# Kernel optimization log

Measured on AMD Instinct MI355X. Metric: run time of the kernel, lower is better.

## Reference

```python
import jax, jax.numpy as jnp
import numpy as np

N = 100000  # num_nodes

def spmm(idx, val, x):
    # sparse [N,N] (COO: idx=[2,E], val=[E]) times dense x [N,F]
    rows, cols = idx[0], idx[1]
    return jax.ops.segment_sum(val[:, None] * x[cols], rows, num_segments=N)


def setup_inputs() -> dict:
    key = jax.random.key(0)
    ks = jax.random.split(key, 12)
    E = 3200000
    F_in, F_out = 128, 128
    inp = {
        "x": jax.random.normal(ks[0], (N, F_in), dtype=jnp.float32),
        "weight": jax.random.normal(ks[1], (F_in, F_out), dtype=jnp.float32) * (1.0 / np.sqrt(F_in)),
        "filter1": 0.9 + 0.2 * jax.random.uniform(ks[2], (N, 1), dtype=jnp.float32),
        "filter2": 0.9 + 0.2 * jax.random.uniform(ks[3], (N, 1), dtype=jnp.float32),
        "filter3": 0.9 + 0.2 * jax.random.uniform(ks[4], (N, 1), dtype=jnp.float32),
        "idx1": jax.random.randint(ks[5], (2, E), 0, N, dtype=jnp.int32),
        "val1": jax.random.normal(ks[6], (E,), dtype=jnp.float32) * 0.01,
        "idx2": jax.random.randint(ks[7], (2, E), 0, N, dtype=jnp.int32),
        "val2": jax.random.normal(ks[8], (E,), dtype=jnp.float32) * 0.01,
        "idx3": jax.random.randint(ks[9], (2, E), 0, N, dtype=jnp.int32),
        "val3": jax.random.normal(ks[10], (E,), dtype=jnp.float32) * 0.01,
    }
    return inp


def reference(x, weight, filter1, filter2, filter3, idx1, val1, idx2, val2, idx3, val3):
    # x = x @ W
    x = x @ weight
    # framelet transform: three spmm branches
    x1 = spmm(idx1, val1, x)
    x2 = spmm(idx2, val2, x)
    x3 = spmm(idx3, val3, x)
    # shrinkage is None -> no-op
    # elementwise learned filters
    x1 = filter1 * x1
    x2 = filter2 * x2
    x3 = filter3 * x3
    # inverse framelet transform
    x1 = spmm(idx1, val1, x1)
    x2 = spmm(idx2, val2, x2)
    x3 = spmm(idx3, val3, x3)
    return x1 + x2 + x3
```

## Files before the change

### kernel.cpp

```cpp
#include <hip/hip_runtime.h>
#include <hip/hip_bf16.h>


#define CHUNK 4096
#define CITER 16
#define MAXC 256

typedef __attribute__((ext_vector_type(8))) short short8;
typedef __attribute__((ext_vector_type(4))) float f32x4;

static __device__ __forceinline__ unsigned short bf16bits(float v) {
  return __builtin_bit_cast(unsigned short, __float2bfloat16(v));
}
static __device__ __forceinline__ float bflo(unsigned u) {
  return __uint_as_float(u << 16);
}
static __device__ __forceinline__ float bfhi(unsigned u) {
  return __uint_as_float(u & 0xffff0000u);
}

__global__ __launch_bounds__(256) void gemm_mfma(const float* __restrict__ x,
                                                 const float* __restrict__ w,
                                                 unsigned short* __restrict__ y,
                                                 int n) {
  __shared__ unsigned short wt[128][136];
  const int tid = threadIdx.x;
#pragma unroll
  for (int it = 0; it < 16; ++it) {
    int i = it * 256 + tid;
    int k = i >> 5;
    int c4 = (i & 31) << 2;
    float4 v = ((const float4*)w)[i];
    wt[c4 + 0][k] = bf16bits(v.x);
    wt[c4 + 1][k] = bf16bits(v.y);
    wt[c4 + 2][k] = bf16bits(v.z);
    wt[c4 + 3][k] = bf16bits(v.w);
  }
  __syncthreads();
  const int lane = tid & 63, wid = tid >> 6;
  const int lr = lane & 15, lq = lane >> 4;
  const int rowbase = blockIdx.x * 128 + wid * 32;
  f32x4 acc[2][8] = {};
#pragma unroll
  for (int ks = 0; ks < 4; ++ks) {
    short8 a[2];
#pragma unroll
    for (int s = 0; s < 2; ++s) {
      int r = rowbase + s * 16 + lr;
      float4 v0 = {0.f, 0.f, 0.f, 0.f}, v1 = {0.f, 0.f, 0.f, 0.f};
      if (r < n) {
        const float* xp = x + (size_t)r * 128 + ks * 32 + lq * 8;
        v0 = *(const float4*)xp;
        v1 = *(const float4*)(xp + 4);
      }
      a[s][0] = bf16bits(v0.x);
      a[s][1] = bf16bits(v0.y);
      a[s][2] = bf16bits(v0.z);
      a[s][3] = bf16bits(v0.w);
      a[s][4] = bf16bits(v1.x);
      a[s][5] = bf16bits(v1.y);
      a[s][6] = bf16bits(v1.z);
      a[s][7] = bf16bits(v1.w);
    }
#pragma unroll
    for (int cs = 0; cs < 8; ++cs) {
      short8 b = *(const short8*)&wt[cs * 16 + lr][ks * 32 + lq * 8];
      acc[0][cs] =
          __builtin_amdgcn_mfma_f32_16x16x32_bf16(a[0], b, acc[0][cs], 0, 0, 0);
      acc[1][cs] =
          __builtin_amdgcn_mfma_f32_16x16x32_bf16(a[1], b, acc[1][cs], 0, 0, 0);
    }
  }
#pragma unroll
  for (int s = 0; s < 2; ++s) {
#pragma unroll
    for (int cs = 0; cs < 8; ++cs) {
      int col = cs * 16 + lr;
      int r0 = rowbase + s * 16 + lq * 4;
#pragma unroll
      for (int j = 0; j < 4; ++j) {
        int r = r0 + j;
        if (r < n) y[(size_t)r * 128 + col] = bf16bits(acc[s][cs][j]);
      }
    }
  }
}

__global__ void ginit(int* __restrict__ gcur, int NC, int CAP) {
  int i = blockIdx.x * 256 + threadIdx.x;
  if (i < NC) gcur[i] = i * CAP;
}

__global__ __launch_bounds__(256) void scatter1(const int* __restrict__ rows,
                                                const int* __restrict__ cols,
                                                const float* __restrict__ vals,
                                                int* __restrict__ gcur,
                                                int2* __restrict__ st1, int E,
                                                int NC) {
  __shared__ int lh[MAXC], gb[MAXC], lc[MAXC];
  __shared__ int rc[CHUNK];
  const int tid = threadIdx.x;
  lh[tid] = 0;
  __syncthreads();
  const int base = blockIdx.x * CHUNK;
#pragma unroll
  for (int k = 0; k < CITER; ++k) {
    int e = base + k * 256 + tid;
    int r = -1;
    if (e < E) {
      r = __builtin_nontemporal_load(rows + e);
      atomicAdd(&lh[r >> 9], 1);
    }
    rc[k * 256 + tid] = r;
  }
  __syncthreads();
  if (tid < NC) {
    int n = lh[tid];
    gb[tid] = n ? atomicAdd(&gcur[tid], n) : 0;
    lc[tid] = 0;
  }
  __syncthreads();
#pragma unroll
  for (int k = 0; k < CITER; ++k) {
    int e = base + k * 256 + tid;
    int r = rc[k * 256 + tid];
    if (r >= 0) {
      int c = r >> 9;
      int off = atomicAdd(&lc[c], 1);
      int2 o;
      o.x = ((r & 511) << 17) | __builtin_nontemporal_load(cols + e);
      o.y = __float_as_int(__builtin_nontemporal_load(vals + e));
      st1[gb[c] + off] = o;
    }
  }
}

__global__ __launch_bounds__(512) void scatter2(const int* __restrict__ gcur,
                                                const int2* __restrict__ st1,
                                                int2* __restrict__ st2,
                                                int2* __restrict__ rowse,
                                                int CAP) {
  __shared__ int sh[512], cur[512];
  const int c = blockIdx.x, tid = threadIdx.x;
  const int a = c * CAP;
  const int b = gcur[c];
  sh[tid] = 0;
  __syncthreads();
  for (int e = a + tid; e < b; e += 512)
    atomicAdd(&sh[(st1[e].x >> 17) & 511], 1);
  __syncthreads();
  int v = sh[tid];
  __syncthreads();
  for (int o = 1; o < 512; o <<= 1) {
    int t2 = (tid >= o) ? sh[tid - o] : 0;
    __syncthreads();
    sh[tid] += t2;
    __syncthreads();
  }
  int end = a + sh[tid];
  int start = end - v;
  cur[tid] = start;
  rowse[c * 512 + tid] = make_int2(start, end);
  __syncthreads();
  for (int e = a + tid; e < b; e += 512) {
    int2 d = st1[e];
    int r = (d.x >> 17) & 511;
    int p = atomicAdd(&cur[r], 1);
    st2[p] = make_int2(d.x & 0x1FFFF, d.y);
  }
}

static __device__ __forceinline__ void row_dot(
    int e, int e1, const int2* __restrict__ edges,
    const unsigned short* __restrict__ src, unsigned loff, float& a0,
    float& a1) {
  for (; e + 7 < e1; e += 8) {
    int4 p0 = *(const int4*)&edges[e];
    int4 p1 = *(const int4*)&edges[e + 2];
    int4 p2 = *(const int4*)&edges[e + 4];
    int4 p3 = *(const int4*)&edges[e + 6];
    unsigned u0 = *(const unsigned*)(src + (((size_t)p0.x) << 7) + loff);
    unsigned u1 = *(const unsigned*)(src + (((size_t)p0.z) << 7) + loff);
    unsigned u2 = *(const unsigned*)(src + (((size_t)p1.x) << 7) + loff);
    unsigned u3 = *(const unsigned*)(src + (((size_t)p1.z) << 7) + loff);
    unsigned u4 = *(const unsigned*)(src + (((size_t)p2.x) << 7) + loff);
    unsigned u5 = *(const unsigned*)(src + (((size_t)p2.z) << 7) + loff);
    unsigned u6 = *(const unsigned*)(src + (((size_t)p3.x) << 7) + loff);
    unsigned u7 = *(const unsigned*)(src + (((size_t)p3.z) << 7) + loff);
    float v0 = __int_as_float(p0.y), v1 = __int_as_float(p0.w);
    float v2 = __int_as_float(p1.y), v3 = __int_as_float(p1.w);
    float v4 = __int_as_float(p2.y), v5 = __int_as_float(p2.w);
    float v6 = __int_as_float(p3.y), v7 = __int_as_float(p3.w);
    a0 += v0 * bflo(u0);
    a1 += v0 * bfhi(u0);
    a0 += v1 * bflo(u1);
    a1 += v1 * bfhi(u1);
    a0 += v2 * bflo(u2);
    a1 += v2 * bfhi(u2);
    a0 += v3 * bflo(u3);
    a1 += v3 * bfhi(u3);
    a0 += v4 * bflo(u4);
    a1 += v4 * bfhi(u4);
    a0 += v5 * bflo(u5);
    a1 += v5 * bfhi(u5);
    a0 += v6 * bflo(u6);
    a1 += v6 * bfhi(u6);
    a0 += v7 * bflo(u7);
    a1 += v7 * bfhi(u7);
  }
  for (; e < e1; ++e) {
    int2 d = edges[e];
    unsigned u = *(const unsigned*)(src + (((size_t)d.x) << 7) + loff);
    float v = __int_as_float(d.y);
    a0 += v * bflo(u);
    a1 += v * bfhi(u);
  }
}

template <int MID>
__global__ __launch_bounds__(256) void spmm_w(
    const int2* __restrict__ rowse, const int2* __restrict__ edges,
    const unsigned short* __restrict__ src, unsigned short* __restrict__ dst,
    float* __restrict__ out, const float* __restrict__ filt, int N, int accm) {
  const int lane = threadIdx.x & 63, wid = threadIdx.x >> 6;
  const int row = blockIdx.x * 4 + wid;
  if (row >= N) return;
  const int2 se = rowse[row];
  float a0 = 0.f, a1 = 0.f;
  const unsigned loff = (unsigned)(lane << 1);
  row_dot(se.x, se.y, edges, src, loff, a0, a1);
  if (MID) {
    float fl = filt[row];
    a0 *= fl;
    a1 *= fl;
    unsigned o = (unsigned)bf16bits(a0) | ((unsigned)bf16bits(a1) << 16);
    *(unsigned*)(dst + ((size_t)row << 7) + loff) = o;
  } else {
    float* op = out + ((size_t)row << 7) + loff;
    float2 r;
    r.x = a0;
    r.y = a1;
    if (accm) {
      float2 c = *(const float2*)op;
      r.x += c.x;
      r.y += c.y;
    }
    *(float2*)op = r;
  }
}

__global__ __launch_bounds__(256) void spmm_out3(
    const int2* __restrict__ rs1, const int2* __restrict__ rs2,
    const int2* __restrict__ rs3, const int2* __restrict__ e1,
    const int2* __restrict__ e2, const int2* __restrict__ e3,
    const unsigned short* __restrict__ t1, const unsigned short* __restrict__ t2,
    const unsigned short* __restrict__ t3, float* __restrict__ out, int N) {
  const int lane = threadIdx.x & 63, wid = threadIdx.x >> 6;
  const int row = blockIdx.x * 4 + wid;
  if (row >= N) return;
  float a0 = 0.f, a1 = 0.f;
  const unsigned loff = (unsigned)(lane << 1);
  int2 s;
  s = rs1[row];
  row_dot(s.x, s.y, e1, t1, loff, a0, a1);
  s = rs2[row];
  row_dot(s.x, s.y, e2, t2, loff, a0, a1);
  s = rs3[row];
  row_dot(s.x, s.y, e3, t3, loff, a0, a1);
  float2 r;
  r.x = a0;
  r.y = a1;
  *(float2*)(out + ((size_t)row << 7) + loff) = r;
}

extern "C" void kernel_launch(void* const* d_in, const int* in_sizes, int n_in,
                              void* d_out, int out_size, void* d_ws, size_t ws_size,
                              hipStream_t stream) {
  const float* x = (const float*)d_in[0];
  const float* w = (const float*)d_in[1];
  const float* filt[3] = {(const float*)d_in[2], (const float*)d_in[3],
                          (const float*)d_in[4]};
  const int* idx[3] = {(const int*)d_in[5], (const int*)d_in[7],
                       (const int*)d_in[9]};
  const float* val[3] = {(const float*)d_in[6], (const float*)d_in[8],
                         (const float*)d_in[10]};
  const int N = in_sizes[2];
  const int E = in_sizes[6];
  float* out = (float*)d_out;

  const int NC = (N + 511) >> 9;
  const int CAP = (((E + NC - 1) / NC) + 2048 + 255) & ~255;
  const size_t NF16 = (size_t)N * 128 * sizeof(unsigned short);
  const size_t STB = (size_t)NC * CAP * 8;
  const size_t RSB = ((size_t)(NC << 9) * 8 + 255) & ~(size_t)255;
  const size_t GCB = (MAXC * 4 + 255) & ~(size_t)255;

  const size_t need_fused = 4 * NF16 + 4 * STB + 3 * RSB + GCB;
  const bool fused = (ws_size >= need_fused);

  char* ws = (char*)d_ws;
  const int gE = (E + CHUNK - 1) / CHUNK;
  const int gS = (N + 3) / 4;

  if (fused) {
    unsigned short* xW = (unsigned short*)ws;
    unsigned short* t[3];
    t[0] = (unsigned short*)(ws + NF16);
    t[1] = (unsigned short*)(ws + 2 * NF16);
    t[2] = (unsigned short*)(ws + 3 * NF16);
    size_t off = 4 * NF16;
    int2* st1 = (int2*)(ws + off);
    off += STB;
    int2* st2[3];
    for (int b = 0; b < 3; ++b) {
      st2[b] = (int2*)(ws + off);
      off += STB;
    }
    int2* rowse[3];
    for (int b = 0; b < 3; ++b) {
      rowse[b] = (int2*)(ws + off);
      off += RSB;
    }
    int* gcur = (int*)(ws + off);

    gemm_mfma<<<(N + 127) / 128, 256, 0, stream>>>(x, w, xW, N);
    for (int b = 0; b < 3; ++b) {
      ginit<<<(NC + 255) / 256, 256, 0, stream>>>(gcur, NC, CAP);
      scatter1<<<gE, 256, 0, stream>>>(idx[b], idx[b] + E, val[b], gcur, st1,
                                       E, NC);
      scatter2<<<NC, 512, 0, stream>>>(gcur, st1, st2[b], rowse[b], CAP);
    }
    for (int b = 0; b < 3; ++b)
      spmm_w<1><<<gS, 256, 0, stream>>>(rowse[b], st2[b], xW, t[b], nullptr,
                                        filt[b], N, 0);
    spmm_out3<<<gS, 256, 0, stream>>>(rowse[0], rowse[1], rowse[2], st2[0],
                                      st2[1], st2[2], t[0], t[1], t[2], out, N);
  } else {
    unsigned short* xW = (unsigned short*)ws;
    unsigned short* t = (unsigned short*)(ws + NF16);
    size_t off = 2 * NF16;
    int2* st1 = (int2*)(ws + off);
    off += STB;
    int2* st2 = (int2*)(ws + off);
    off += STB;
    int2* rowse = (int2*)(ws + off);
    off += RSB;
    int* gcur = (int*)(ws + off);

    gemm_mfma<<<(N + 127) / 128, 256, 0, stream>>>(x, w, xW, N);
    for (int b = 0; b < 3; ++b) {
      ginit<<<(NC + 255) / 256, 256, 0, stream>>>(gcur, NC, CAP);
      scatter1<<<gE, 256, 0, stream>>>(idx[b], idx[b] + E, val[b], gcur, st1,
                                       E, NC);
      scatter2<<<NC, 512, 0, stream>>>(gcur, st1, st2, rowse, CAP);
      spmm_w<1><<<gS, 256, 0, stream>>>(rowse, st2, xW, t, nullptr, filt[b], N,
                                        0);
      spmm_w<0><<<gS, 256, 0, stream>>>(rowse, st2, t, nullptr, out, nullptr,
                                        N, b > 0 ? 1 : 0);
    }
  }
}
```

Before: 1.027 ms.

## Fuse three forward SpMM branches, sort edges by column bucket, merge gcur init

New measurement: 1.041 ms. No clear change (+1.5%).

```diff
diff --git a/kernel.cpp b/kernel.cpp
--- a/kernel.cpp
+++ b/kernel.cpp
@@ -86,9 +86,9 @@
   }
 }
 
-__global__ void ginit(int* __restrict__ gcur, int NC, int CAP) {
+__global__ void ginit3(int* __restrict__ gcur, int NC, int CAP) {
   int i = blockIdx.x * 256 + threadIdx.x;
-  if (i < NC) gcur[i] = i * CAP;
+  if (i < 3 * NC) gcur[(i / NC) * MAXC + (i % NC)] = (i % NC) * CAP;
 }
 
 __global__ __launch_bounds__(256) void scatter1(const int* __restrict__ rows,
@@ -140,32 +140,45 @@
                                                 int2* __restrict__ st2,
                                                 int2* __restrict__ rowse,
                                                 int CAP) {
-  __shared__ int sh[512], cur[512];
+  __shared__ int cnt[4096], cur[4096], ssc[512];
   const int c = blockIdx.x, tid = threadIdx.x;
   const int a = c * CAP;
   const int b = gcur[c];
-  sh[tid] = 0;
-  __syncthreads();
-  for (int e = a + tid; e < b; e += 512)
-    atomicAdd(&sh[(st1[e].x >> 17) & 511], 1);
-  __syncthreads();
-  int v = sh[tid];
+  for (int i = tid; i < 4096; i += 512) cnt[i] = 0;
+  __syncthreads();
+  for (int e = a + tid; e < b; e += 512) {
+    int x = st1[e].x;
+    atomicAdd(&cnt[(((x >> 17) & 511) << 3) | ((x >> 14) & 7)], 1);
+  }
+  __syncthreads();
+  const int base = tid << 3;
+  int loc[8], s = 0;
+#pragma unroll
+  for (int j = 0; j < 8; ++j) {
+    loc[j] = cnt[base + j];
+    s += loc[j];
+  }
+  ssc[tid] = s;
   __syncthreads();
   for (int o = 1; o < 512; o <<= 1) {
-    int t2 = (tid >= o) ? sh[tid - o] : 0;
+    int t2 = (tid >= o) ? ssc[tid - o] : 0;
     __syncthreads();
-    sh[tid] += t2;
+    ssc[tid] += t2;
     __syncthreads();
   }
-  int end = a + sh[tid];
-  int start = end - v;
-  cur[tid] = start;
-  rowse[c * 512 + tid] = make_int2(start, end);
+  int ex = ssc[tid] - s;
+  int run = ex;
+#pragma unroll
+  for (int j = 0; j < 8; ++j) {
+    cur[base + j] = a + run;
+    run += loc[j];
+  }
+  rowse[(c << 9) + tid] = make_int2(a + ex, a + ex + s);
   __syncthreads();
   for (int e = a + tid; e < b; e += 512) {
     int2 d = st1[e];
-    int r = (d.x >> 17) & 511;
-    int p = atomicAdd(&cur[r], 1);
+    int bin = (((d.x >> 17) & 511) << 3) | ((d.x >> 14) & 7);
+    int p = atomicAdd(&cur[bin], 1);
     st2[p] = make_int2(d.x & 0x1FFFF, d.y);
   }
 }
@@ -249,6 +262,42 @@
   }
 }
 
+__global__ __launch_bounds__(256) void spmm_mid3(
+    const int2* __restrict__ rs0, const int2* __restrict__ rs1,
+    const int2* __restrict__ rs2, const int2* __restrict__ e0,
+    const int2* __restrict__ e1, const int2* __restrict__ e2,
+    const unsigned short* __restrict__ xW, unsigned short* __restrict__ t0,
+    unsigned short* __restrict__ t1, unsigned short* __restrict__ t2,
+    const float* __restrict__ f0, const float* __restrict__ f1,
+    const float* __restrict__ f2, int N) {
+  const int lane = threadIdx.x & 63, wid = threadIdx.x >> 6;
+  const int row = blockIdx.x * 4 + wid;
+  if (row >= N) return;
+  const unsigned loff = (unsigned)(lane << 1);
+  const size_t po = ((size_t)row << 7) + loff;
+  int2 s;
+  float a0, a1, fl;
+  unsigned o;
+  s = rs0[row];
+  a0 = a1 = 0.f;
+  row_dot(s.x, s.y, e0, xW, loff, a0, a1);
+  fl = f0[row];
+  o = (unsigned)bf16bits(a0 * fl) | ((unsigned)bf16bits(a1 * fl) << 16);
+  *(unsigned*)(t0 + po) = o;
+  s = rs1[row];
+  a0 = a1 = 0.f;
+  row_dot(s.x, s.y, e1, xW, loff, a0, a1);
+  fl = f1[row];
+  o = (unsigned)bf16bits(a0 * fl) | ((unsigned)bf16bits(a1 * fl) << 16);
+  *(unsigned*)(t1 + po) = o;
+  s = rs2[row];
+  a0 = a1 = 0.f;
+  row_dot(s.x, s.y, e2, xW, loff, a0, a1);
+  fl = f2[row];
+  o = (unsigned)bf16bits(a0 * fl) | ((unsigned)bf16bits(a1 * fl) << 16);
+  *(unsigned*)(t2 + po) = o;
+}
+
 __global__ __launch_bounds__(256) void spmm_out3(
     const int2* __restrict__ rs1, const int2* __restrict__ rs2,
     const int2* __restrict__ rs3, const int2* __restrict__ e1,
@@ -293,7 +342,7 @@
   const size_t NF16 = (size_t)N * 128 * sizeof(unsigned short);
   const size_t STB = (size_t)NC * CAP * 8;
   const size_t RSB = ((size_t)(NC << 9) * 8 + 255) & ~(size_t)255;
-  const size_t GCB = (MAXC * 4 + 255) & ~(size_t)255;
+  const size_t GCB = (3 * MAXC * 4 + 255) & ~(size_t)255;
 
   const size_t need_fused = 4 * NF16 + 4 * STB + 3 * RSB + GCB;
   const bool fused = (ws_size >= need_fused);
@@ -323,16 +372,17 @@
     }
     int* gcur = (int*)(ws + off);
 
+    ginit3<<<(3 * NC + 255) / 256, 256, 0, stream>>>(gcur, NC, CAP);
     gemm_mfma<<<(N + 127) / 128, 256, 0, stream>>>(x, w, xW, N);
     for (int b = 0; b < 3; ++b) {
-      ginit<<<(NC + 255) / 256, 256, 0, stream>>>(gcur, NC, CAP);
-      scatter1<<<gE, 256, 0, stream>>>(idx[b], idx[b] + E, val[b], gcur, st1,
-                                       E, NC);
-      scatter2<<<NC, 512, 0, stream>>>(gcur, st1, st2[b], rowse[b], CAP);
-    }
-    for (int b = 0; b < 3; ++b)
-      spmm_w<1><<<gS, 256, 0, stream>>>(rowse[b], st2[b], xW, t[b], nullptr,
-                                        filt[b], N, 0);
+      scatter1<<<gE, 256, 0, stream>>>(idx[b], idx[b] + E, val[b],
+                                       gcur + b * MAXC, st1, E, NC);
+      scatter2<<<NC, 512, 0, stream>>>(gcur + b * MAXC, st1, st2[b], rowse[b],
+                                       CAP);
+    }
+    spmm_mid3<<<gS, 256, 0, stream>>>(rowse[0], rowse[1], rowse[2], st2[0],
+                                      st2[1], st2[2], xW, t[0], t[1], t[2],
+                                      filt[0], filt[1], filt[2], N);
     spmm_out3<<<gS, 256, 0, stream>>>(rowse[0], rowse[1], rowse[2], st2[0],
                                       st2[1], st2[2], t[0], t[1], t[2], out, N);
   } else {
@@ -347,12 +397,12 @@
     off += RSB;
     int* gcur = (int*)(ws + off);
 
+    ginit3<<<(3 * NC + 255) / 256, 256, 0, stream>>>(gcur, NC, CAP);
     gemm_mfma<<<(N + 127) / 128, 256, 0, stream>>>(x, w, xW, N);
     for (int b = 0; b < 3; ++b) {
-      ginit<<<(NC + 255) / 256, 256, 0, stream>>>(gcur, NC, CAP);
-      scatter1<<<gE, 256, 0, stream>>>(idx[b], idx[b] + E, val[b], gcur, st1,
-                                       E, NC);
-      scatter2<<<NC, 512, 0, stream>>>(gcur, st1, st2, rowse, CAP);
+      scatter1<<<gE, 256, 0, stream>>>(idx[b], idx[b] + E, val[b],
+                                       gcur + b * MAXC, st1, E, NC);
+      scatter2<<<NC, 512, 0, stream>>>(gcur + b * MAXC, st1, st2, rowse, CAP);
       spmm_w<1><<<gS, 256, 0, stream>>>(rowse, st2, xW, t, nullptr, filt[b], N,
                                         0);
       spmm_w<0><<<gS, 256, 0, stream>>>(rowse, st2, t, nullptr, out, nullptr,
```
